# Optimization experiments

Measured on AMD Instinct MI355X. Metric: run time of the kernel, lower is better.

Reference implementation:

```python
import jax, jax.numpy as jnp
import numpy as np

SEQ, BATCH, IN, HID, OUT = 1024, 2048, 32, 12, 1


def setup_inputs() -> dict:
    key = jax.random.key(0)
    ks = jax.random.split(key, 12)
    s = 0.1
    return {
        "X": jax.random.normal(ks[0], (SEQ, BATCH, IN), dtype=jnp.float32),
        # layer 0 (PyTorch gate order: i, f, g, o)
        "Wih0": jax.random.normal(ks[1], (4 * HID, IN), dtype=jnp.float32) * s,
        "Whh0": jax.random.normal(ks[2], (4 * HID, HID), dtype=jnp.float32) * s,
        "bih0": jax.random.normal(ks[3], (4 * HID,), dtype=jnp.float32) * s,
        "bhh0": jax.random.normal(ks[4], (4 * HID,), dtype=jnp.float32) * s,
        # layer 1
        "Wih1": jax.random.normal(ks[5], (4 * HID, HID), dtype=jnp.float32) * s,
        "Whh1": jax.random.normal(ks[6], (4 * HID, HID), dtype=jnp.float32) * s,
        "bih1": jax.random.normal(ks[7], (4 * HID,), dtype=jnp.float32) * s,
        "bhh1": jax.random.normal(ks[8], (4 * HID,), dtype=jnp.float32) * s,
        # final linear head
        "Wfc": jax.random.normal(ks[9], (OUT, HID), dtype=jnp.float32) * s,
        "bfc": jax.random.normal(ks[10], (OUT,), dtype=jnp.float32) * s,
    }


def _lstm_layer(xs, Wih, Whh, bih, bhh):
    # xs: [S, B, D] seq-first, PyTorch nn.LSTM semantics (gate order i,f,g,o)
    B = xs.shape[1]
    H = Whh.shape[1]
    h0 = jnp.zeros((B, H), xs.dtype)
    c0 = jnp.zeros((B, H), xs.dtype)
    b = bih + bhh

    def step(carry, x_t):
        h, c = carry
        z = x_t @ Wih.T + h @ Whh.T + b  # [B, 4H]
        i, f, g, o = jnp.split(z, 4, axis=-1)
        c = jax.nn.sigmoid(f) * c + jax.nn.sigmoid(i) * jnp.tanh(g)
        h = jax.nn.sigmoid(o) * jnp.tanh(c)
        return (h, c), h

    _, hs = jax.lax.scan(step, (h0, c0), xs)
    return hs  # [S, B, H]


def reference(X, Wih0, Whh0, bih0, bhh0, Wih1, Whh1, bih1, bhh1, Wfc, bfc):
    out = _lstm_layer(X, Wih0, Whh0, bih0, bhh0)
    out = _lstm_layer(out, Wih1, Whh1, bih1, bhh1)
    # faithful to original: out[:, -1, :] on seq-first output selects the
    # LAST BATCH element for every timestep -> [S, H]
    last = out[:, -1, :]
    return last @ Wfc.T + bfc  # [S, OUT]
```

## Files before the change

### kernel.cpp

```cpp
#include <hip/hip_runtime.h>

#define SEQ    1024
#define NBATCH 2048
#define INDIM  32
#define HID    12
#define G4     48
#define NB     (SEQ / 4)
#define CHUNK  16
#define NCH    (SEQ / CHUNK)

#define LOG2E 1.4426950408889634f

typedef float f32x2 __attribute__((ext_vector_type(2)));
typedef float f32x4 __attribute__((ext_vector_type(4)));

template<int CTRL>
__device__ __forceinline__ float qbcast(float v) {
    int x = __builtin_amdgcn_update_dpp(
        0, __builtin_bit_cast(int, v), CTRL, 0xF, 0xF, true);
    return __builtin_bit_cast(float, x);
}
__device__ __forceinline__ float lanebcast(float v, int lane) {
    return __builtin_bit_cast(float,
        __builtin_amdgcn_readlane(__builtin_bit_cast(int, v), lane));
}

__global__ __launch_bounds__(256) void lstm_pre(
    const float* __restrict__ X,
    const float* __restrict__ Wih0,
    const float* __restrict__ bih0,
    const float* __restrict__ bhh0,
    float* __restrict__ zx)
{
    int idx = blockIdx.x * blockDim.x + threadIdx.x;
    if (idx >= (NB + 2) * 192) return;
    int b   = idx / 192;
    int rem = idx - b * 192;
    int j   = rem >> 2;
    int q   = rem & 3;
    int t   = 4 * b + q;
    if (t >= SEQ) { zx[idx] = 0.0f; return; }
    int g = j & 3, k = j >> 2;
    int r = g * HID + k;
    const float cexpg = (g == 2) ? (-2.0f * LOG2E) : (-LOG2E);
    const float* x = X + (size_t)t * NBATCH * INDIM + (size_t)(NBATCH - 1) * INDIM;
    const float* w = Wih0 + r * INDIM;
    float za = bih0[r] + bhh0[r], zb = 0.0f;
    #pragma unroll
    for (int kk = 0; kk < INDIM; kk += 2) {
        za = fmaf(w[kk],     x[kk],     za);
        zb = fmaf(w[kk + 1], x[kk + 1], zb);
    }
    zx[idx] = (za + zb) * cexpg;
}

__global__ __launch_bounds__(128) void lstm_seq2(
    const f32x4* __restrict__ zx4,
    float* __restrict__ hbuf,
    const float* __restrict__ Whh0,
    const float* __restrict__ Wih1,
    const float* __restrict__ Whh1,
    const float* __restrict__ bih1,
    const float* __restrict__ bhh1)
{
    __shared__ alignas(16) float lds_h0[(SEQ + 4) * HID];
    __shared__ int done;

    const int tid  = threadIdx.x;
    const int wave = tid >> 6;
    const int lane = tid & 63;
    const int jj = (lane < G4) ? lane : 0;
    const int g  = jj & 3;
    const int k  = jj >> 2;
    const int r  = g * HID + k;
    const float cexp = (g == 2) ? (-2.0f * LOG2E) : (-LOG2E);

    if (tid == 0) done = 0;
    __syncthreads();

    if (wave == 0) {
        if (lane < 4 * HID) lds_h0[SEQ * HID + lane] = 0.0f;

        f32x2 wh0[HID / 2];
        #pragma unroll
        for (int kk = 0; kk < HID / 2; ++kk)
            wh0[kk] = f32x2{Whh0[r * HID + 2 * kk] * cexp,
                            Whh0[r * HID + 2 * kk + 1] * cexp};

        f32x2 ph0[HID / 2];
        #pragma unroll
        for (int kk = 0; kk < HID / 2; ++kk) ph0[kk] = f32x2{0.f, 0.f};
        float c0 = 0.0f;

        auto step = [&](float zs, int t) {
            f32x2 a0 = f32x2{zs, 0.f}, a1 = f32x2{0.f, 0.f};
            #pragma unroll
            for (int kk = 0; kk < HID / 2; kk += 2) {
                a0 = __builtin_elementwise_fma(wh0[kk],     ph0[kk],     a0);
                a1 = __builtin_elementwise_fma(wh0[kk + 1], ph0[kk + 1], a1);
            }
            float z  = (a0.x + a1.x) + (a0.y + a1.y);
            float e  = __builtin_amdgcn_exp2f(z);
            float rr = __builtin_amdgcn_rcpf(1.0f + e);
            float ai = qbcast<0x00>(rr);
            float af = qbcast<0x55>(rr);
            float ag = qbcast<0xAA>(rr);
            float ao = qbcast<0xFF>(rr);
            c0 = fmaf(af, c0, fmaf(ai + ai, ag, -ai));
            float e2 = __builtin_amdgcn_exp2f(c0 * (-2.0f * LOG2E));
            float rt = __builtin_amdgcn_rcpf(1.0f + e2);
            float h0 = fmaf(ao + ao, rt, -ao);
            if (lane < G4 && g == 0) lds_h0[t * HID + k] = h0;
            #pragma unroll
            for (int kk = 0; kk < HID / 2; ++kk) {
                ph0[kk].x = lanebcast(h0, 8 * kk);
                ph0[kk].y = lanebcast(h0, 8 * kk + 4);
            }
        };

        f32x4 cur = zx4[jj];
        f32x4 nxt = zx4[G4 + jj];
        f32x4 fut = zx4[2 * G4 + jj];
        step(cur.x, 0); step(cur.y, 1); step(cur.z, 2); step(cur.w, 3);
        for (int b = 1; b < NB; ++b) {
            cur = nxt; nxt = fut;
            fut = zx4[(b + 2) * G4 + jj];
            int t = 4 * b;
            step(cur.x, t); step(cur.y, t + 1);
            step(cur.z, t + 2); step(cur.w, t + 3);
            if ((b & 3) == 3)
                __hip_atomic_store(&done, (b >> 2) + 1,
                                   __ATOMIC_RELEASE, __HIP_MEMORY_SCOPE_WORKGROUP);
        }
    } else {
        f32x2 wi1[HID / 2], wh1[HID / 2];
        #pragma unroll
        for (int kk = 0; kk < HID / 2; ++kk) {
            wi1[kk] = f32x2{Wih1[r * HID + 2 * kk] * cexp,
                            Wih1[r * HID + 2 * kk + 1] * cexp};
            wh1[kk] = f32x2{Whh1[r * HID + 2 * kk] * cexp,
                            Whh1[r * HID + 2 * kk + 1] * cexp};
        }
        const float b1s = (bih1[r] + bhh1[r]) * cexp;

        f32x2 ph1[HID / 2];
        #pragma unroll
        for (int kk = 0; kk < HID / 2; ++kk) ph1[kk] = f32x2{0.f, 0.f};
        float c1 = 0.0f;

        auto l1z = [&](const f32x2* h0c) {
            f32x2 a0 = f32x2{b1s, 0.f}, a1 = f32x2{0.f, 0.f};
            f32x2 a2 = f32x2{0.f, 0.f},  a3 = f32x2{0.f, 0.f};
            #pragma unroll
            for (int kk = 0; kk < HID / 2; kk += 2) {
                a0 = __builtin_elementwise_fma(wi1[kk],     h0c[kk],     a0);
                a1 = __builtin_elementwise_fma(wi1[kk + 1], h0c[kk + 1], a1);
                a2 = __builtin_elementwise_fma(wh1[kk],     ph1[kk],     a2);
                a3 = __builtin_elementwise_fma(wh1[kk + 1], ph1[kk + 1], a3);
            }
            f32x2 s = (a0 + a1) + (a2 + a3);
            return s.x + s.y;
        };

        auto l1fin = [&](float z1, int t) {
            float e  = __builtin_amdgcn_exp2f(z1);
            float rr = __builtin_amdgcn_rcpf(1.0f + e);
            float ai = qbcast<0x00>(rr);
            float af = qbcast<0x55>(rr);
            float ag = qbcast<0xAA>(rr);
            float ao = qbcast<0xFF>(rr);
            c1 = fmaf(af, c1, fmaf(ai + ai, ag, -ai));
            float e2 = __builtin_amdgcn_exp2f(c1 * (-2.0f * LOG2E));
            float rt = __builtin_amdgcn_rcpf(1.0f + e2);
            float h1 = fmaf(ao + ao, rt, -ao);
            if (lane < G4 && g == 0) hbuf[t * HID + k] = h1;
            #pragma unroll
            for (int kk = 0; kk < HID / 2; ++kk) {
                ph1[kk].x = lanebcast(h1, 8 * kk);
                ph1[kk].y = lanebcast(h1, 8 * kk + 4);
            }
        };

        auto ldsld = [&](int t, f32x2* dst) {
            #pragma unroll
            for (int kk = 0; kk < HID / 2; ++kk)
                dst[kk] = *reinterpret_cast<const f32x2*>(&lds_h0[t * HID + 2 * kk]);
        };

        int seen = 0;
        do {
            seen = __hip_atomic_load(&done, __ATOMIC_ACQUIRE,
                                     __HIP_MEMORY_SCOPE_WORKGROUP);
        } while (seen < 2);

        f32x2 cA[HID / 2], cB[HID / 2], nA[HID / 2], nBv[HID / 2];
        ldsld(0, cA);
        ldsld(1, cB);

        for (int c = 0; c < NCH; ++c) {
            int need = (c + 2 < NCH) ? (c + 2) : NCH;
            if (seen < need) {
                do {
                    __builtin_amdgcn_s_sleep(2);
                    seen = __hip_atomic_load(&done, __ATOMIC_ACQUIRE,
                                             __HIP_MEMORY_SCOPE_WORKGROUP);
                } while (seen < need);
            }
            int t0 = c * CHUNK;
            #pragma unroll
            for (int p = 0; p < CHUNK / 2; ++p) {
                int t = t0 + 2 * p;
                float z1a = l1z(cA);
                ldsld(t + 2, nA);
                l1fin(z1a, t);
                float z1b = l1z(cB);
                ldsld(t + 3, nBv);
                l1fin(z1b, t + 1);
                #pragma unroll
                for (int kk = 0; kk < HID / 2; ++kk) { cA[kk] = nA[kk]; cB[kk] = nBv[kk]; }
            }
        }
    }
}

__global__ __launch_bounds__(256) void fc_head(
    const float* __restrict__ hbuf,
    const float* __restrict__ Wfc,
    const float* __restrict__ bfc,
    float* __restrict__ out)
{
    int t = blockIdx.x * blockDim.x + threadIdx.x;
    if (t >= SEQ) return;
    float o = bfc[0];
    const float* h = hbuf + t * HID;
    #pragma unroll
    for (int kk = 0; kk < HID; ++kk) o = fmaf(Wfc[kk], h[kk], o);
    out[t] = o;
}

__global__ __launch_bounds__(64) void lstm_seq_fb(
    const float* __restrict__ X,
    const float* __restrict__ Wih0,
    const float* __restrict__ bih0,
    const float* __restrict__ bhh0,
    const float* __restrict__ Whh0,
    const float* __restrict__ Wih1,
    const float* __restrict__ Whh1,
    const float* __restrict__ bih1,
    const float* __restrict__ bhh1,
    const float* __restrict__ Wfc,
    const float* __restrict__ bfc,
    float* __restrict__ out)
{
    const int j  = threadIdx.x;
    const int jj = (j < G4) ? j : 0;
    const int g  = jj & 3;
    const int k  = jj >> 2;
    const int r  = g * HID + k;
    const float cexp = (g == 2) ? (-2.0f * LOG2E) : (-LOG2E);

    float whh0[HID], wih1[HID], whh1[HID], wih0[INDIM], wfc[HID];
    #pragma unroll
    for (int kk = 0; kk < HID; ++kk) {
        whh0[kk] = Whh0[r * HID + kk] * cexp;
        wih1[kk] = Wih1[r * HID + kk] * cexp;
        whh1[kk] = Whh1[r * HID + kk] * cexp;
        wfc[kk]  = Wfc[kk];
    }
    #pragma unroll
    for (int kk = 0; kk < INDIM; ++kk) wih0[kk] = Wih0[r * INDIM + kk] * cexp;
    const float b0 = (bih0[r] + bhh0[r]) * cexp;
    const float b1 = (bih1[r] + bhh1[r]) * cexp;
    const float bias_fc = bfc[0];

    float h0v[HID], h1v[HID];
    #pragma unroll
    for (int kk = 0; kk < HID; ++kk) { h0v[kk] = 0.0f; h1v[kk] = 0.0f; }
    float c0 = 0.0f, c1 = 0.0f;

    for (int t = 0; t < SEQ; ++t) {
        const float* x = X + (size_t)t * NBATCH * INDIM
                           + (size_t)(NBATCH - 1) * INDIM;
        float z0 = b0;
        #pragma unroll
        for (int kk = 0; kk < INDIM; ++kk) z0 = fmaf(wih0[kk], x[kk], z0);
        #pragma unroll
        for (int kk = 0; kk < HID; ++kk) z0 = fmaf(whh0[kk], h0v[kk], z0);
        float e  = __builtin_amdgcn_exp2f(z0);
        float rr = __builtin_amdgcn_rcpf(1.0f + e);
        float ai = qbcast<0x00>(rr), af = qbcast<0x55>(rr);
        float ag = qbcast<0xAA>(rr), ao = qbcast<0xFF>(rr);
        c0 = fmaf(af, c0, fmaf(ai + ai, ag, -ai));
        float e2 = __builtin_amdgcn_exp2f(c0 * (-2.0f * LOG2E));
        float rt = __builtin_amdgcn_rcpf(1.0f + e2);
        float h0 = fmaf(ao + ao, rt, -ao);
        #pragma unroll
        for (int kk = 0; kk < HID; ++kk) h0v[kk] = lanebcast(h0, 4 * kk);

        float z1 = b1;
        #pragma unroll
        for (int kk = 0; kk < HID; ++kk) {
            z1 = fmaf(wih1[kk], h0v[kk], z1);
            z1 = fmaf(whh1[kk], h1v[kk], z1);
        }
        e  = __builtin_amdgcn_exp2f(z1);
        rr = __builtin_amdgcn_rcpf(1.0f + e);
        ai = qbcast<0x00>(rr); af = qbcast<0x55>(rr);
        ag = qbcast<0xAA>(rr); ao = qbcast<0xFF>(rr);
        c1 = fmaf(af, c1, fmaf(ai + ai, ag, -ai));
        e2 = __builtin_amdgcn_exp2f(c1 * (-2.0f * LOG2E));
        rt = __builtin_amdgcn_rcpf(1.0f + e2);
        float h1 = fmaf(ao + ao, rt, -ao);
        #pragma unroll
        for (int kk = 0; kk < HID; ++kk) h1v[kk] = lanebcast(h1, 4 * kk);

        float o = bias_fc;
        #pragma unroll
        for (int kk = 0; kk < HID; ++kk) o = fmaf(wfc[kk], h1v[kk], o);
        if (j == 0) out[t] = o;
    }
}

extern "C" void kernel_launch(void* const* d_in, const int* in_sizes, int n_in,
                              void* d_out, int out_size, void* d_ws, size_t ws_size,
                              hipStream_t stream) {
    const float* X    = (const float*)d_in[0];
    const float* Wih0 = (const float*)d_in[1];
    const float* Whh0 = (const float*)d_in[2];
    const float* bih0 = (const float*)d_in[3];
    const float* bhh0 = (const float*)d_in[4];
    const float* Wih1 = (const float*)d_in[5];
    const float* Whh1 = (const float*)d_in[6];
    const float* bih1 = (const float*)d_in[7];
    const float* bhh1 = (const float*)d_in[8];
    const float* Wfc  = (const float*)d_in[9];
    const float* bfc  = (const float*)d_in[10];
    float* out = (float*)d_out;

    const size_t zx_floats = (size_t)(NB + 2) * 192;
    const size_t need = (zx_floats + (size_t)SEQ * HID) * sizeof(float);
    if (ws_size >= need) {
        float* zbuf = (float*)d_ws;
        float* hbuf = zbuf + zx_floats;
        lstm_pre<<<((NB + 2) * 192 + 255) / 256, 256, 0, stream>>>(
            X, Wih0, bih0, bhh0, zbuf);
        lstm_seq2<<<1, 128, 0, stream>>>(
            (const f32x4*)zbuf, hbuf, Whh0, Wih1, Whh1, bih1, bhh1);
        fc_head<<<(SEQ + 255) / 256, 256, 0, stream>>>(hbuf, Wfc, bfc, out);
    } else {
        lstm_seq_fb<<<1, 64, 0, stream>>>(
            X, Wih0, bih0, bhh0, Whh0,
            Wih1, Whh1, bih1, bhh1, Wfc, bfc, out);
    }
}
```

Before: 155.4 us.

## Replace spin-wait flag with lockstep barrier pipeline between LSTM layer waves

The two-wave layer pipeline no longer uses an LDS atomic flag with polling and sleep. Instead both waves run a shared loop with __syncthreads per 16-step chunk, and layer 1 lags layer 0 by two chunks. Matvecs move to f32x4 vectors, the zx prefetch is widened to whole chunks, and the cell update is rescaled so the tanh of c needs one fewer multiply on the serial chain. The price is a per-chunk barrier that can stall the faster wave, plus higher register use from the larger prefetch buffers.

```diff
diff --git a/kernel.cpp b/kernel.cpp
--- a/kernel.cpp
+++ b/kernel.cpp
@@ -6,6 +6,7 @@
 #define HID    12
 #define G4     48
 #define NB     (SEQ / 4)
+#define NBLK   (NB + 4)
 #define CHUNK  16
 #define NCH    (SEQ / CHUNK)
 
@@ -23,6 +24,9 @@
 __device__ __forceinline__ float lanebcast(float v, int lane) {
     return __builtin_bit_cast(float,
         __builtin_amdgcn_readlane(__builtin_bit_cast(int, v), lane));
+}
+__device__ __forceinline__ float sig_part(float zs) {
+    return __builtin_amdgcn_rcpf(1.0f + __builtin_amdgcn_exp2f(zs));
 }
 
 __global__ __launch_bounds__(256) void lstm_pre(
@@ -33,7 +37,7 @@
     float* __restrict__ zx)
 {
     int idx = blockIdx.x * blockDim.x + threadIdx.x;
-    if (idx >= (NB + 2) * 192) return;
+    if (idx >= NBLK * 192) return;
     int b   = idx / 192;
     int rem = idx - b * 192;
     int j   = rem >> 2;
@@ -64,7 +68,6 @@
     const float* __restrict__ bhh1)
 {
     __shared__ alignas(16) float lds_h0[(SEQ + 4) * HID];
-    __shared__ int done;
 
     const int tid  = threadIdx.x;
     const int wave = tid >> 6;
@@ -74,153 +77,135 @@
     const int k  = jj >> 2;
     const int r  = g * HID + k;
     const float cexp = (g == 2) ? (-2.0f * LOG2E) : (-LOG2E);
-
-    if (tid == 0) done = 0;
+    const float TSA = -4.0f * LOG2E;
+    const float TSB =  2.0f * LOG2E;
+
+    f32x4 wh0[3];
+    f32x4 zbE[4], zbO[4];
+    f32x4 ph0[3];  float cs0 = 0.0f;
+    f32x4 wi1[3], wh1[3];
+    f32x4 hb0[4][3], hb1[4][3];
+    f32x4 ph1[3];  float cs1 = 0.0f;
+    float b1s = 0.0f;
+
+    #pragma unroll
+    for (int m = 0; m < 3; ++m) { ph0[m] = f32x4{0,0,0,0}; ph1[m] = f32x4{0,0,0,0}; }
+
+    if (wave == 0) {
+        if (lane < G4) lds_h0[SEQ * HID + lane] = 0.0f;
+        #pragma unroll
+        for (int m = 0; m < 3; ++m)
+            wh0[m] = *(const f32x4*)(Whh0 + r * HID + 4 * m) * cexp;
+        #pragma unroll
+        for (int bb = 0; bb < 4; ++bb) zbE[bb] = zx4[bb * G4 + jj];
+    } else {
+        #pragma unroll
+        for (int m = 0; m < 3; ++m) {
+            wi1[m] = *(const f32x4*)(Wih1 + r * HID + 4 * m) * cexp;
+            wh1[m] = *(const f32x4*)(Whh1 + r * HID + 4 * m) * cexp;
+        }
+        b1s = (bih1[r] + bhh1[r]) * cexp;
+    }
     __syncthreads();
 
-    if (wave == 0) {
-        if (lane < 4 * HID) lds_h0[SEQ * HID + lane] = 0.0f;
-
-        f32x2 wh0[HID / 2];
-        #pragma unroll
-        for (int kk = 0; kk < HID / 2; ++kk)
-            wh0[kk] = f32x2{Whh0[r * HID + 2 * kk] * cexp,
-                            Whh0[r * HID + 2 * kk + 1] * cexp};
-
-        f32x2 ph0[HID / 2];
-        #pragma unroll
-        for (int kk = 0; kk < HID / 2; ++kk) ph0[kk] = f32x2{0.f, 0.f};
-        float c0 = 0.0f;
-
-        auto step = [&](float zs, int t) {
-            f32x2 a0 = f32x2{zs, 0.f}, a1 = f32x2{0.f, 0.f};
-            #pragma unroll
-            for (int kk = 0; kk < HID / 2; kk += 2) {
-                a0 = __builtin_elementwise_fma(wh0[kk],     ph0[kk],     a0);
-                a1 = __builtin_elementwise_fma(wh0[kk + 1], ph0[kk + 1], a1);
+#define STEPA(zs, t) { \
+    f32x4 a0 = __builtin_elementwise_fma(wh0[0], ph0[0], f32x4{(zs), 0.f, 0.f, 0.f}); \
+    f32x4 a1 = __builtin_elementwise_fma(wh0[1], ph0[1], f32x4{0.f, 0.f, 0.f, 0.f}); \
+    f32x4 a2 = __builtin_elementwise_fma(wh0[2], ph0[2], f32x4{0.f, 0.f, 0.f, 0.f}); \
+    f32x4 sv = (a0 + a1) + a2; \
+    float z  = (sv.x + sv.y) + (sv.z + sv.w); \
+    float rr = sig_part(z); \
+    float ai = qbcast<0x00>(rr), af = qbcast<0x55>(rr); \
+    float ag = qbcast<0xAA>(rr), ao = qbcast<0xFF>(rr); \
+    float igs = ai * fmaf(TSA, ag, TSB); \
+    cs0 = fmaf(af, cs0, igs); \
+    float rt = sig_part(cs0); \
+    float h0 = fmaf(ao + ao, rt, -ao); \
+    if (lane < G4 && g == 0) lds_h0[(t) * HID + k] = h0; \
+    ph0[0] = f32x4{lanebcast(h0, 0),  lanebcast(h0, 4),  lanebcast(h0, 8),  lanebcast(h0, 12)}; \
+    ph0[1] = f32x4{lanebcast(h0, 16), lanebcast(h0, 20), lanebcast(h0, 24), lanebcast(h0, 28)}; \
+    ph0[2] = f32x4{lanebcast(h0, 32), lanebcast(h0, 36), lanebcast(h0, 40), lanebcast(h0, 44)}; \
+}
+
+#define AITER(cur, nxt, ci) { \
+    int cb = 4 * ((ci) + 1); \
+    nxt[0] = zx4[(cb + 0) * G4 + jj]; \
+    nxt[1] = zx4[(cb + 1) * G4 + jj]; \
+    nxt[2] = zx4[(cb + 2) * G4 + jj]; \
+    nxt[3] = zx4[(cb + 3) * G4 + jj]; \
+    int tA = CHUNK * (ci); \
+    STEPA(cur[0].x, tA + 0)  STEPA(cur[0].y, tA + 1)  STEPA(cur[0].z, tA + 2)  STEPA(cur[0].w, tA + 3)  \
+    STEPA(cur[1].x, tA + 4)  STEPA(cur[1].y, tA + 5)  STEPA(cur[1].z, tA + 6)  STEPA(cur[1].w, tA + 7)  \
+    STEPA(cur[2].x, tA + 8)  STEPA(cur[2].y, tA + 9)  STEPA(cur[2].z, tA + 10) STEPA(cur[2].w, tA + 11) \
+    STEPA(cur[3].x, tA + 12) STEPA(cur[3].y, tA + 13) STEPA(cur[3].z, tA + 14) STEPA(cur[3].w, tA + 15) \
+}
+
+#define LDGRP(trow, dst) { \
+    dst[0][0] = *(const f32x4*)&lds_h0[((trow) + 0) * HID + 0]; \
+    dst[0][1] = *(const f32x4*)&lds_h0[((trow) + 0) * HID + 4]; \
+    dst[0][2] = *(const f32x4*)&lds_h0[((trow) + 0) * HID + 8]; \
+    dst[1][0] = *(const f32x4*)&lds_h0[((trow) + 1) * HID + 0]; \
+    dst[1][1] = *(const f32x4*)&lds_h0[((trow) + 1) * HID + 4]; \
+    dst[1][2] = *(const f32x4*)&lds_h0[((trow) + 1) * HID + 8]; \
+    dst[2][0] = *(const f32x4*)&lds_h0[((trow) + 2) * HID + 0]; \
+    dst[2][1] = *(const f32x4*)&lds_h0[((trow) + 2) * HID + 4]; \
+    dst[2][2] = *(const f32x4*)&lds_h0[((trow) + 2) * HID + 8]; \
+    dst[3][0] = *(const f32x4*)&lds_h0[((trow) + 3) * HID + 0]; \
+    dst[3][1] = *(const f32x4*)&lds_h0[((trow) + 3) * HID + 4]; \
+    dst[3][2] = *(const f32x4*)&lds_h0[((trow) + 3) * HID + 8]; \
+}
+
+#define STEPB(cur, qi, t) { \
+    f32x4 a0 = __builtin_elementwise_fma(wi1[0], cur[qi][0], f32x4{b1s, 0.f, 0.f, 0.f}); \
+    f32x4 a1 = __builtin_elementwise_fma(wi1[1], cur[qi][1], f32x4{0.f, 0.f, 0.f, 0.f}); \
+    f32x4 a2 = __builtin_elementwise_fma(wi1[2], cur[qi][2], f32x4{0.f, 0.f, 0.f, 0.f}); \
+    a0 = __builtin_elementwise_fma(wh1[0], ph1[0], a0); \
+    a1 = __builtin_elementwise_fma(wh1[1], ph1[1], a1); \
+    a2 = __builtin_elementwise_fma(wh1[2], ph1[2], a2); \
+    f32x4 sv = (a0 + a1) + a2; \
+    float z  = (sv.x + sv.y) + (sv.z + sv.w); \
+    float rr = sig_part(z); \
+    float ai = qbcast<0x00>(rr), af = qbcast<0x55>(rr); \
+    float ag = qbcast<0xAA>(rr), ao = qbcast<0xFF>(rr); \
+    float igs = ai * fmaf(TSA, ag, TSB); \
+    cs1 = fmaf(af, cs1, igs); \
+    float rt = sig_part(cs1); \
+    float h1 = fmaf(ao + ao, rt, -ao); \
+    if (lane < G4 && g == 0) hbuf[(t) * HID + k] = h1; \
+    ph1[0] = f32x4{lanebcast(h1, 0),  lanebcast(h1, 4),  lanebcast(h1, 8),  lanebcast(h1, 12)}; \
+    ph1[1] = f32x4{lanebcast(h1, 16), lanebcast(h1, 20), lanebcast(h1, 24), lanebcast(h1, 28)}; \
+    ph1[2] = f32x4{lanebcast(h1, 32), lanebcast(h1, 36), lanebcast(h1, 40), lanebcast(h1, 44)}; \
+}
+
+#define BGRP(cur, nxt, tload, tproc) { \
+    LDGRP((tload), nxt) \
+    STEPB(cur, 0, (tproc) + 0) STEPB(cur, 1, (tproc) + 1) \
+    STEPB(cur, 2, (tproc) + 2) STEPB(cur, 3, (tproc) + 3) \
+}
+
+    for (int i = 0; i < NCH + 2; ++i) {
+        if (wave == 0) {
+            if (i < NCH) {
+                if ((i & 1) == 0) { AITER(zbE, zbO, i) }
+                else              { AITER(zbO, zbE, i) }
             }
-            float z  = (a0.x + a1.x) + (a0.y + a1.y);
-            float e  = __builtin_amdgcn_exp2f(z);
-            float rr = __builtin_amdgcn_rcpf(1.0f + e);
-            float ai = qbcast<0x00>(rr);
-            float af = qbcast<0x55>(rr);
-            float ag = qbcast<0xAA>(rr);
-            float ao = qbcast<0xFF>(rr);
-            c0 = fmaf(af, c0, fmaf(ai + ai, ag, -ai));
-            float e2 = __builtin_amdgcn_exp2f(c0 * (-2.0f * LOG2E));
-            float rt = __builtin_amdgcn_rcpf(1.0f + e2);
-            float h0 = fmaf(ao + ao, rt, -ao);
-            if (lane < G4 && g == 0) lds_h0[t * HID + k] = h0;
-            #pragma unroll
-            for (int kk = 0; kk < HID / 2; ++kk) {
-                ph0[kk].x = lanebcast(h0, 8 * kk);
-                ph0[kk].y = lanebcast(h0, 8 * kk + 4);
-            }
-        };
-
-        f32x4 cur = zx4[jj];
-        f32x4 nxt = zx4[G4 + jj];
-        f32x4 fut = zx4[2 * G4 + jj];
-        step(cur.x, 0); step(cur.y, 1); step(cur.z, 2); step(cur.w, 3);
-        for (int b = 1; b < NB; ++b) {
-            cur = nxt; nxt = fut;
-            fut = zx4[(b + 2) * G4 + jj];
-            int t = 4 * b;
-            step(cur.x, t); step(cur.y, t + 1);
-            step(cur.z, t + 2); step(cur.w, t + 3);
-            if ((b & 3) == 3)
-                __hip_atomic_store(&done, (b >> 2) + 1,
-                                   __ATOMIC_RELEASE, __HIP_MEMORY_SCOPE_WORKGROUP);
-        }
-    } else {
-        f32x2 wi1[HID / 2], wh1[HID / 2];
-        #pragma unroll
-        for (int kk = 0; kk < HID / 2; ++kk) {
-            wi1[kk] = f32x2{Wih1[r * HID + 2 * kk] * cexp,
-                            Wih1[r * HID + 2 * kk + 1] * cexp};
-            wh1[kk] = f32x2{Whh1[r * HID + 2 * kk] * cexp,
-                            Whh1[r * HID + 2 * kk + 1] * cexp};
-        }
-        const float b1s = (bih1[r] + bhh1[r]) * cexp;
-
-        f32x2 ph1[HID / 2];
-        #pragma unroll
-        for (int kk = 0; kk < HID / 2; ++kk) ph1[kk] = f32x2{0.f, 0.f};
-        float c1 = 0.0f;
-
-        auto l1z = [&](const f32x2* h0c) {
-            f32x2 a0 = f32x2{b1s, 0.f}, a1 = f32x2{0.f, 0.f};
-            f32x2 a2 = f32x2{0.f, 0.f},  a3 = f32x2{0.f, 0.f};
-            #pragma unroll
-            for (int kk = 0; kk < HID / 2; kk += 2) {
-                a0 = __builtin_elementwise_fma(wi1[kk],     h0c[kk],     a0);
-                a1 = __builtin_elementwise_fma(wi1[kk + 1], h0c[kk + 1], a1);
-                a2 = __builtin_elementwise_fma(wh1[kk],     ph1[kk],     a2);
-                a3 = __builtin_elementwise_fma(wh1[kk + 1], ph1[kk + 1], a3);
-            }
-            f32x2 s = (a0 + a1) + (a2 + a3);
-            return s.x + s.y;
-        };
-
-        auto l1fin = [&](float z1, int t) {
-            float e  = __builtin_amdgcn_exp2f(z1);
-            float rr = __builtin_amdgcn_rcpf(1.0f + e);
-            float ai = qbcast<0x00>(rr);
-            float af = qbcast<0x55>(rr);
-            float ag = qbcast<0xAA>(rr);
-            float ao = qbcast<0xFF>(rr);
-            c1 = fmaf(af, c1, fmaf(ai + ai, ag, -ai));
-            float e2 = __builtin_amdgcn_exp2f(c1 * (-2.0f * LOG2E));
-            float rt = __builtin_amdgcn_rcpf(1.0f + e2);
-            float h1 = fmaf(ao + ao, rt, -ao);
-            if (lane < G4 && g == 0) hbuf[t * HID + k] = h1;
-            #pragma unroll
-            for (int kk = 0; kk < HID / 2; ++kk) {
-                ph1[kk].x = lanebcast(h1, 8 * kk);
-                ph1[kk].y = lanebcast(h1, 8 * kk + 4);
-            }
-        };
-
-        auto ldsld = [&](int t, f32x2* dst) {
-            #pragma unroll
-            for (int kk = 0; kk < HID / 2; ++kk)
-                dst[kk] = *reinterpret_cast<const f32x2*>(&lds_h0[t * HID + 2 * kk]);
-        };
-
-        int seen = 0;
-        do {
-            seen = __hip_atomic_load(&done, __ATOMIC_ACQUIRE,
-                                     __HIP_MEMORY_SCOPE_WORKGROUP);
-        } while (seen < 2);
-
-        f32x2 cA[HID / 2], cB[HID / 2], nA[HID / 2], nBv[HID / 2];
-        ldsld(0, cA);
-        ldsld(1, cB);
-
-        for (int c = 0; c < NCH; ++c) {
-            int need = (c + 2 < NCH) ? (c + 2) : NCH;
-            if (seen < need) {
-                do {
-                    __builtin_amdgcn_s_sleep(2);
-                    seen = __hip_atomic_load(&done, __ATOMIC_ACQUIRE,
-                                             __HIP_MEMORY_SCOPE_WORKGROUP);
-                } while (seen < need);
-            }
-            int t0 = c * CHUNK;
-            #pragma unroll
-            for (int p = 0; p < CHUNK / 2; ++p) {
-                int t = t0 + 2 * p;
-                float z1a = l1z(cA);
-                ldsld(t + 2, nA);
-                l1fin(z1a, t);
-                float z1b = l1z(cB);
-                ldsld(t + 3, nBv);
-                l1fin(z1b, t + 1);
-                #pragma unroll
-                for (int kk = 0; kk < HID / 2; ++kk) { cA[kk] = nA[kk]; cB[kk] = nBv[kk]; }
+        } else {
+            if (i >= 2) {
+                int t0 = (i - 2) * CHUNK;
+                if (i == 2) { LDGRP(0, hb0) }
+                BGRP(hb0, hb1, t0 + 4,  t0)
+                BGRP(hb1, hb0, t0 + 8,  t0 + 4)
+                BGRP(hb0, hb1, t0 + 12, t0 + 8)
+                BGRP(hb1, hb0, t0 + 16, t0 + 12)
             }
         }
-    }
+        __syncthreads();
+    }
+#undef STEPA
+#undef AITER
+#undef LDGRP
+#undef STEPB
+#undef BGRP
 }
 
 __global__ __launch_bounds__(256) void fc_head(
@@ -258,6 +243,8 @@
     const int k  = jj >> 2;
     const int r  = g * HID + k;
     const float cexp = (g == 2) ? (-2.0f * LOG2E) : (-LOG2E);
+    const float TSA = -4.0f * LOG2E;
+    const float TSB =  2.0f * LOG2E;
 
     float whh0[HID], wih1[HID], whh1[HID], wih0[INDIM], wfc[HID];
     #pragma unroll
@@ -276,7 +263,7 @@
     float h0v[HID], h1v[HID];
     #pragma unroll
     for (int kk = 0; kk < HID; ++kk) { h0v[kk] = 0.0f; h1v[kk] = 0.0f; }
-    float c0 = 0.0f, c1 = 0.0f;
+    float cs0 = 0.0f, cs1 = 0.0f;
 
     for (int t = 0; t < SEQ; ++t) {
         const float* x = X + (size_t)t * NBATCH * INDIM
@@ -286,13 +273,11 @@
         for (int kk = 0; kk < INDIM; ++kk) z0 = fmaf(wih0[kk], x[kk], z0);
         #pragma unroll
         for (int kk = 0; kk < HID; ++kk) z0 = fmaf(whh0[kk], h0v[kk], z0);
-        float e  = __builtin_amdgcn_exp2f(z0);
-        float rr = __builtin_amdgcn_rcpf(1.0f + e);
+        float rr = sig_part(z0);
         float ai = qbcast<0x00>(rr), af = qbcast<0x55>(rr);
         float ag = qbcast<0xAA>(rr), ao = qbcast<0xFF>(rr);
-        c0 = fmaf(af, c0, fmaf(ai + ai, ag, -ai));
-        float e2 = __builtin_amdgcn_exp2f(c0 * (-2.0f * LOG2E));
-        float rt = __builtin_amdgcn_rcpf(1.0f + e2);
+        cs0 = fmaf(af, cs0, ai * fmaf(TSA, ag, TSB));
+        float rt = sig_part(cs0);
         float h0 = fmaf(ao + ao, rt, -ao);
         #pragma unroll
         for (int kk = 0; kk < HID; ++kk) h0v[kk] = lanebcast(h0, 4 * kk);
@@ -303,13 +288,11 @@
             z1 = fmaf(wih1[kk], h0v[kk], z1);
             z1 = fmaf(whh1[kk], h1v[kk], z1);
         }
-        e  = __builtin_amdgcn_exp2f(z1);
-        rr = __builtin_amdgcn_rcpf(1.0f + e);
+        rr = sig_part(z1);
         ai = qbcast<0x00>(rr); af = qbcast<0x55>(rr);
         ag = qbcast<0xAA>(rr); ao = qbcast<0xFF>(rr);
-        c1 = fmaf(af, c1, fmaf(ai + ai, ag, -ai));
-        e2 = __builtin_amdgcn_exp2f(c1 * (-2.0f * LOG2E));
-        rt = __builtin_amdgcn_rcpf(1.0f + e2);
+        cs1 = fmaf(af, cs1, ai * fmaf(TSA, ag, TSB));
+        rt = sig_part(cs1);
         float h1 = fmaf(ao + ao, rt, -ao);
         #pragma unroll
         for (int kk = 0; kk < HID; ++kk) h1v[kk] = lanebcast(h1, 4 * kk);
@@ -337,12 +320,12 @@
     const float* bfc  = (const float*)d_in[10];
     float* out = (float*)d_out;
 
-    const size_t zx_floats = (size_t)(NB + 2) * 192;
+    const size_t zx_floats = (size_t)NBLK * 192;
     const size_t need = (zx_floats + (size_t)SEQ * HID) * sizeof(float);
     if (ws_size >= need) {
         float* zbuf = (float*)d_ws;
         float* hbuf = zbuf + zx_floats;
-        lstm_pre<<<((NB + 2) * 192 + 255) / 256, 256, 0, stream>>>(
+        lstm_pre<<<(NBLK * 192 + 255) / 256, 256, 0, stream>>>(
             X, Wih0, bih0, bhh0, zbuf);
         lstm_seq2<<<1, 128, 0, stream>>>(
             (const f32x4*)zbuf, hbuf, Whh0, Wih1, Whh1, bih1, bhh1);
```

Result: no change. 153.6 us (-1.2%).
